# Optimization experiments

Hardware: AMD Instinct MI355X
Metric: run time of the kernel (lower is better)

Reference implementation:

```python
import jax, jax.numpy as jnp
import numpy as np
import math

B, T = 16, 512
P = 256          # num_memory_positions
E = 128          # embedding_dim
NB = 4           # num_beings
K = 4            # attention_radius
TEMP = 8.0       # attention_temperature
PHI = 1.618033988749895


def setup_inputs() -> dict:
    key = jax.random.key(0)
    ks = jax.random.split(key, 8)
    x = jax.random.normal(ks[0], (B, T, 8), jnp.float32)
    W_in = jax.random.normal(ks[1], (8, E), jnp.float32) * 0.1
    b_in = jnp.zeros((E,), jnp.float32)
    W_out = jax.random.normal(ks[2], (E, 8), jnp.float32) * 0.1
    b_out = jnp.zeros((8,), jnp.float32)
    W_p = jax.random.normal(ks[3], (E, E), jnp.float32) * (1.0 / np.sqrt(E))
    b_p = jnp.zeros((E,), jnp.float32)
    ptr_dest = jax.random.uniform(ks[4], (NB, P), jnp.float32) * P
    jump_W = jax.random.normal(ks[5], (NB, E), jnp.float32) * 0.1
    jump_b = jnp.zeros((NB,), jnp.float32)
    ctx_strength = jnp.full((NB,), 0.2, jnp.float32)
    pe = np.zeros((NB, E), np.float32)
    for i in range(NB):
        ph = i * PHI
        v = []
        for h in range(1, 9):
            v += [math.sin(h * ph), math.cos(h * ph)]
        pe[i, :16] = v  # phase_embedding padded with zeros to E (E >= 16)
    phase_bias = jnp.asarray(pe)
    seg = P / NB
    pointer_init = jax.random.uniform(ks[6], (NB, B), jnp.float32) * seg + jnp.arange(NB, dtype=jnp.float32)[:, None] * seg
    return dict(x=x, W_in=W_in, b_in=b_in, W_out=W_out, b_out=b_out,
                W_p=W_p, b_p=b_p, ptr_dest=ptr_dest, jump_W=jump_W,
                jump_b=jump_b, ctx_strength=ctx_strength,
                phase_bias=phase_bias, pointer_init=pointer_init)


def _forward(x, W_in, b_in, W_out, b_out, W_p, b_p, ptr_dest, jump_W,
             jump_b, ctx_strength, phase_bias, pointer_init):
    offsets = jnp.arange(-K, K + 1)          # [W]
    b_ix = jnp.arange(B)                     # [B]
    half = P / 2.0
    ring0 = jnp.zeros((B, P, E), x.dtype)
    hid0 = jnp.zeros((NB, B, E), x.dtype)

    def step(carry, x_t):
        ring, ptrs, hids = carry
        inp = x_t @ W_in + b_in              # [B,E]
        outs, new_ptrs, new_hids = [], [], []
        for i in range(NB):                  # beings sequential (share ring)
            ptr, hid = ptrs[i], hids[i]
            base = jnp.clip(jnp.floor(ptr).astype(jnp.int32), 0, P - 1)
            idx = (base[:, None] + offsets[None, :]) % P            # [B,W]
            delta = jnp.mod(idx.astype(x_t.dtype) - ptr[:, None] + half, P) - half
            w = jax.nn.softmax(-(delta ** 2) / TEMP, axis=1)         # [B,W]
            nbhd = ring[b_ix[:, None], idx]                          # [B,W,E]
            ctx = jnp.sum(w[..., None] * nbhd, axis=1)               # [B,E]
            comb = inp + jax.nn.sigmoid(ctx_strength[i]) * ctx + 0.1 * phase_bias[i]
            s = jnp.tanh(comb + hid)
            s = jnp.tanh(s @ W_p + b_p)      # depth-1 = 1 processing layer
            ring = ring.at[b_ix[:, None], idx].add(w[..., None] * s[:, None, :])
            cur = jnp.clip(ptr.astype(jnp.int32), 0, P - 1)
            jump_target = ptr_dest[i][cur]                           # [B]
            probs = jax.nn.sigmoid(s @ jump_W[i] + jump_b[i])        # [B]
            hard = (probs > 0.5).astype(s.dtype)
            should_jump = hard - jax.lax.stop_gradient(probs) + probs
            walk = (ptr + 1.0) % P
            new_ptrs.append(jnp.where(should_jump > 0.5, jump_target, walk))
            new_hids.append(s)
            outs.append(s @ W_out + b_out)                           # [B,8]
        out_t = jnp.mean(jnp.stack(outs), axis=0)                    # [B,8] (training-mode mean)
        return (ring, jnp.stack(new_ptrs), jnp.stack(new_hids)), out_t

    _, ys = jax.lax.scan(step, (ring0, pointer_init, hid0), jnp.swapaxes(x, 0, 1))
    return jnp.swapaxes(ys, 0, 1)            # [B,T,8]


def reference(x, W_in, b_in, W_out, b_out, W_p, b_p, ptr_dest, jump_W,
              jump_b, ctx_strength, phase_bias, pointer_init):
    return _forward(x, W_in, b_in, W_out, b_out, W_p, b_p, ptr_dest,
                    jump_W, jump_b, ctx_strength, phase_bias, pointer_init)
```

## Files before the change

kernel.cpp:

```cpp
#include <hip/hip_runtime.h>
#include <cmath>

namespace {
constexpr int B_ = 16, T_ = 512, P_ = 256, E_ = 128, NB_ = 4, K_ = 4;

__device__ __forceinline__ float rcpf(float x) { return __builtin_amdgcn_rcpf(x); }
__device__ __forceinline__ float fast_tanh(float x) {
    float a = fabsf(x);
    float t = __expf(-2.0f * a);
    float r = 1.0f - 2.0f * t * rcpf(1.0f + t);
    return copysignf(r, x);
}
__device__ __forceinline__ float redkq(float v) {
    v += __shfl_xor(v, 16);
    v += __shfl_xor(v, 32);
    return v;
}
__device__ __forceinline__ float sel4(int kq, float a, float b, float c, float d) {
    const float t0 = (kq & 1) ? b : a;
    const float t1 = (kq & 1) ? d : c;
    return (kq & 2) ? t1 : t0;
}
}

__global__ __launch_bounds__(256, 1)
void swarm_ring_kernel(const float* __restrict__ x,
                       const float* __restrict__ W_in,
                       const float* __restrict__ b_in,
                       const float* __restrict__ W_out,
                       const float* __restrict__ b_out,
                       const float* __restrict__ W_p,
                       const float* __restrict__ b_p,
                       const float* __restrict__ ptr_dest,
                       const float* __restrict__ jump_W,
                       const float* __restrict__ jump_b,
                       const float* __restrict__ ctx_strength,
                       const float* __restrict__ phase_bias,
                       const float* __restrict__ pointer_init,
                       float* __restrict__ out)
{
    __shared__ alignas(16) float  ring[P_ * E_];
    __shared__ alignas(16) float4 s4[E_];
    __shared__ alignas(16) float  sbuf[2 * E_];
    __shared__ alignas(16) float  red[16];
    __shared__ alignas(16) float  hist[16][132];
    __shared__ alignas(16) float  wout_s[8][132];

    const int tid = threadIdx.x;
    const int b   = blockIdx.x;
    const int w   = tid >> 6;
    const int l   = tid & 63;
    const int sub = l & 15;
    const int kq  = l >> 4;
    const int e0  = ((w << 4) | sub) << 1;

    for (int k4 = tid; k4 < P_ * E_ / 4; k4 += 256)
        ((float4*)ring)[k4] = make_float4(0.f, 0.f, 0.f, 0.f);
    for (int idx = tid; idx < 8 * E_; idx += 256) {
        const int m = idx >> 7, ee = idx & 127;
        wout_s[m][ee] = W_out[ee * 8 + m] * 0.25f;
    }

    float2 wp2[32];
    #pragma unroll
    for (int kk = 0; kk < 32; ++kk)
        wp2[kk] = *(const float2*)(W_p + (kq * 32 + kk) * E_ + e0);

    const float2 bin2 = *(const float2*)(b_in + e0);
    const float2 bp2  = *(const float2*)(b_p + e0);
    const float  bout_m = b_out[tid & 7];

    float2 pb2[NB_], jw2[NB_], hid2[NB_];
    float  sigc[NB_], jb_r[NB_], ptrv[NB_];
    #pragma unroll
    for (int i = 0; i < NB_; ++i) {
        const float2 pb = *(const float2*)(phase_bias + i * E_ + e0);
        pb2[i] = make_float2(0.1f * pb.x, 0.1f * pb.y);
        jw2[i] = *(const float2*)(jump_W + i * E_ + e0);
        sigc[i] = 1.0f / (1.0f + __expf(-ctx_strength[i]));
        jb_r[i] = jump_b[i];
        hid2[i] = make_float2(0.f, 0.f);
        ptrv[i] = pointer_init[i * B_ + b];
    }

    const float* xb = x + (size_t)b * T_ * 8;
    float xt[8];
    {
        float4 a0 = ((const float4*)xb)[0], a1 = ((const float4*)xb)[1];
        xt[0]=a0.x; xt[1]=a0.y; xt[2]=a0.z; xt[3]=a0.w;
        xt[4]=a1.x; xt[5]=a1.y; xt[6]=a1.z; xt[7]=a1.w;
    }

    const float Cw1 = 0.8824969f, Cw2 = 0.60653066f, Cw3 = 0.32465247f, Cw4 = 0.13533528f;
    const float Dw1 = 0.7788008f, Dw2 = 0.36787944f, Dw3 = 0.105399225f, Dw4 = 0.018315639f;

    __syncthreads();

    for (int t = 0; t < T_; ++t) {
        int   baseA[NB_];
        float fA[NB_], psinv[NB_], jt[NB_], wgt[NB_][9];
        #pragma unroll
        for (int i = 0; i < NB_; ++i) {
            const float p = ptrv[i];
            const int base = (int)p;
            baseA[i] = base;
            jt[i] = ptr_dest[i * P_ + base];
            const float f = p - (float)base;
            fA[i] = f;
            const float r  = __expf(0.25f * f);
            const float r2 = r * r, r3 = r2 * r, r4 = r2 * r2;
            const float ri = rcpf(r), ri2 = ri * ri, ri3 = ri2 * ri, ri4 = ri2 * ri2;
            const float p0 = Cw4*ri4, p1 = Cw3*ri3, p2 = Cw2*ri2, p3 = Cw1*ri, p4 = 1.0f,
                        p5 = Cw1*r,  p6 = Cw2*r2,  p7 = Cw3*r3,  p8 = Cw4*r4;
            const float sum = ((p0+p1)+(p2+p3)) + ((p4+p5)+(p6+p7)) + p8;
            const float inv = rcpf(sum);
            psinv[i] = inv;
            wgt[i][0]=p0*inv; wgt[i][1]=p1*inv; wgt[i][2]=p2*inv; wgt[i][3]=p3*inv;
            wgt[i][4]=p4*inv; wgt[i][5]=p5*inv; wgt[i][6]=p6*inv; wgt[i][7]=p7*inv;
            wgt[i][8]=p8*inv;
        }

        int ddm[NB_][NB_];
        bool overlap = false;
        #pragma unroll
        for (int j = 1; j < NB_; ++j)
            #pragma unroll
            for (int i = 0; i < j; ++i) {
                const int dd = ((baseA[j] - baseA[i] + 128) & 255) - 128;
                ddm[j][i] = dd;
                overlap = overlap || (dd >= -8 && dd <= 8);
            }

        float  ws0[NB_], ws1[NB_];
        float2 ctxp2[NB_];
        #pragma unroll
        for (int i = 0; i < NB_; ++i) {
            ws0[i] = sel4(kq, wgt[i][0], wgt[i][1], wgt[i][2], wgt[i][3]);
            ws1[i] = sel4(kq, wgt[i][4], wgt[i][5], wgt[i][6], wgt[i][7]);
            const int r0 = (baseA[i] + kq - K_) & (P_ - 1);
            const int r1 = (baseA[i] + kq + 4 - K_) & (P_ - 1);
            const float2 g0 = *(const float2*)(ring + r0 * E_ + e0);
            const float2 g1 = *(const float2*)(ring + r1 * E_ + e0);
            float cx = fmaf(ws1[i], g1.x, ws0[i] * g0.x);
            float cy = fmaf(ws1[i], g1.y, ws0[i] * g0.y);
            if (kq == 0) {
                const int r2 = (baseA[i] + 8 - K_) & (P_ - 1);
                const float2 g2 = *(const float2*)(ring + r2 * E_ + e0);
                cx = fmaf(wgt[i][8], g2.x, cx);
                cy = fmaf(wgt[i][8], g2.y, cy);
            }
            ctxp2[i] = make_float2(redkq(cx), redkq(cy));
        }

        float2 inp2 = bin2;
        #pragma unroll
        for (int k = 0; k < 8; ++k) {
            const float2 wk = *(const float2*)(W_in + k * E_ + e0);
            inp2.x = fmaf(xt[k], wk.x, inp2.x);
            inp2.y = fmaf(xt[k], wk.y, inp2.y);
        }

        float xtn[8];
        if (t + 1 < T_) {
            float4 a0 = ((const float4*)(xb + (t + 1) * 8))[0];
            float4 a1 = ((const float4*)(xb + (t + 1) * 8))[1];
            xtn[0]=a0.x; xtn[1]=a0.y; xtn[2]=a0.z; xtn[3]=a0.w;
            xtn[4]=a1.x; xtn[5]=a1.y; xtn[6]=a1.z; xtn[7]=a1.w;
        } else {
            #pragma unroll
            for (int k = 0; k < 8; ++k) xtn[k] = 0.f;
        }

        float2 sv2[NB_];

        if (!overlap) {
            float2 s1v[NB_];
            #pragma unroll
            for (int j = 0; j < NB_; ++j) {
                s1v[j].x = fast_tanh(fmaf(sigc[j], ctxp2[j].x, inp2.x + pb2[j].x + hid2[j].x));
                s1v[j].y = fast_tanh(fmaf(sigc[j], ctxp2[j].y, inp2.y + pb2[j].y + hid2[j].y));
            }
            if (kq == 0) {
                s4[e0]     = make_float4(s1v[0].x, s1v[1].x, s1v[2].x, s1v[3].x);
                s4[e0 + 1] = make_float4(s1v[0].y, s1v[1].y, s1v[2].y, s1v[3].y);
            }
            __syncthreads();

            float2 ab0 = make_float2(0.f, 0.f), ab1 = ab0, ab2 = ab0, ab3 = ab0;
            const float4* sp = s4 + kq * 32;
            #pragma unroll
            for (int kk = 0; kk < 32; ++kk) {
                const float4 sq = sp[kk];
                const float2 w2 = wp2[kk];
                ab0.x = fmaf(sq.x, w2.x, ab0.x); ab0.y = fmaf(sq.x, w2.y, ab0.y);
                ab1.x = fmaf(sq.y, w2.x, ab1.x); ab1.y = fmaf(sq.y, w2.y, ab1.y);
                ab2.x = fmaf(sq.z, w2.x, ab2.x); ab2.y = fmaf(sq.z, w2.y, ab2.y);
                ab3.x = fmaf(sq.w, w2.x, ab3.x); ab3.y = fmaf(sq.w, w2.y, ab3.y);
            }
            sv2[0] = make_float2(fast_tanh(redkq(ab0.x) + bp2.x), fast_tanh(redkq(ab0.y) + bp2.y));
            sv2[1] = make_float2(fast_tanh(redkq(ab1.x) + bp2.x), fast_tanh(redkq(ab1.y) + bp2.y));
            sv2[2] = make_float2(fast_tanh(redkq(ab2.x) + bp2.x), fast_tanh(redkq(ab2.y) + bp2.y));
            sv2[3] = make_float2(fast_tanh(redkq(ab3.x) + bp2.x), fast_tanh(redkq(ab3.y) + bp2.y));
            #pragma unroll
            for (int j = 0; j < NB_; ++j) hid2[j] = sv2[j];

            #pragma unroll
            for (int j = 0; j < NB_; ++j) {
                const float2 s = sv2[j];
                const int r0 = (baseA[j] + kq - K_) & (P_ - 1);
                float2* q0 = (float2*)(ring + r0 * E_ + e0);
                float2 v0 = *q0;
                v0.x = fmaf(ws0[j], s.x, v0.x); v0.y = fmaf(ws0[j], s.y, v0.y);
                *q0 = v0;
                const int r1 = (baseA[j] + kq + 4 - K_) & (P_ - 1);
                float2* q1 = (float2*)(ring + r1 * E_ + e0);
                float2 v1 = *q1;
                v1.x = fmaf(ws1[j], s.x, v1.x); v1.y = fmaf(ws1[j], s.y, v1.y);
                *q1 = v1;
                if (kq == 0) {
                    const int r2 = (baseA[j] + 8 - K_) & (P_ - 1);
                    float2* q2 = (float2*)(ring + r2 * E_ + e0);
                    float2 v2 = *q2;
                    v2.x = fmaf(wgt[j][8], s.x, v2.x); v2.y = fmaf(wgt[j][8], s.y, v2.y);
                    *q2 = v2;
                }
            }
        } else {
            float coefm[NB_][NB_];
            #pragma unroll
            for (int j = 1; j < NB_; ++j) {
                #pragma unroll
                for (int i = 0; i < j; ++i) {
                    const int dd = ddm[j][i];
                    float c = 0.f;
                    if (dd >= -8 && dd <= 8) {
                        const float A = (float)dd - fA[i];
                        const float s  = __expf(-0.25f * (A - fA[j]));
                        const float G  = __expf(0.125f * (fA[i] * fA[i] - A * A));
                        const float s2p = s * s, s3p = s2p * s, s4p = s2p * s2p;
                        const float si = rcpf(s), si2 = si * si, si3 = si2 * si, si4 = si2 * si2;
                        float acc = 0.f;
                        acc += (dd >= 0)              ? Dw4 * si4 : 0.f;
                        acc += (dd >= -1 && dd <= 7)  ? Dw3 * si3 : 0.f;
                        acc += (dd >= -2 && dd <= 6)  ? Dw2 * si2 : 0.f;
                        acc += (dd >= -3 && dd <= 5)  ? Dw1 * si  : 0.f;
                        acc += (dd >= -4 && dd <= 4)  ? 1.0f      : 0.f;
                        acc += (dd >= -5 && dd <= 3)  ? Dw1 * s   : 0.f;
                        acc += (dd >= -6 && dd <= 2)  ? Dw2 * s2p : 0.f;
                        acc += (dd >= -7 && dd <= 1)  ? Dw3 * s3p : 0.f;
                        acc += (dd <= 0)              ? Dw4 * s4p : 0.f;
                        c = psinv[i] * psinv[j] * G * acc;
                    }
                    coefm[j][i] = c;
                }
            }

            #pragma unroll
            for (int j = 0; j < NB_; ++j) {
                float2 ctx = ctxp2[j];
                #pragma unroll
                for (int i = 0; i < j; ++i) {
                    ctx.x = fmaf(coefm[j][i], sv2[i].x, ctx.x);
                    ctx.y = fmaf(coefm[j][i], sv2[i].y, ctx.y);
                }
                float2 s1;
                s1.x = fast_tanh(fmaf(sigc[j], ctx.x, inp2.x + pb2[j].x + hid2[j].x));
                s1.y = fast_tanh(fmaf(sigc[j], ctx.y, inp2.y + pb2[j].y + hid2[j].y));
                if (kq == 0) *(float2*)(sbuf + (j & 1) * E_ + e0) = s1;
                __syncthreads();

                const float4* sp = (const float4*)(sbuf + (j & 1) * E_) + kq * 8;
                float ax = 0.f, ay = 0.f;
                #pragma unroll
                for (int kk = 0; kk < 8; ++kk) {
                    const float4 sq = sp[kk];
                    const float2 wa = wp2[4 * kk + 0], wb = wp2[4 * kk + 1];
                    const float2 wc = wp2[4 * kk + 2], wd = wp2[4 * kk + 3];
                    ax = fmaf(sq.x, wa.x, ax); ay = fmaf(sq.x, wa.y, ay);
                    ax = fmaf(sq.y, wb.x, ax); ay = fmaf(sq.y, wb.y, ay);
                    ax = fmaf(sq.z, wc.x, ax); ay = fmaf(sq.z, wc.y, ay);
                    ax = fmaf(sq.w, wd.x, ax); ay = fmaf(sq.w, wd.y, ay);
                }
                float2 s2;
                s2.x = fast_tanh(redkq(ax) + bp2.x);
                s2.y = fast_tanh(redkq(ay) + bp2.y);
                sv2[j] = s2; hid2[j] = s2;

                const int r0 = (baseA[j] + kq - K_) & (P_ - 1);
                float2* q0 = (float2*)(ring + r0 * E_ + e0);
                float2 v0 = *q0;
                v0.x = fmaf(ws0[j], s2.x, v0.x); v0.y = fmaf(ws0[j], s2.y, v0.y);
                *q0 = v0;
                const int r1 = (baseA[j] + kq + 4 - K_) & (P_ - 1);
                float2* q1 = (float2*)(ring + r1 * E_ + e0);
                float2 v1 = *q1;
                v1.x = fmaf(ws1[j], s2.x, v1.x); v1.y = fmaf(ws1[j], s2.y, v1.y);
                *q1 = v1;
                if (kq == 0) {
                    const int r2 = (baseA[j] + 8 - K_) & (P_ - 1);
                    float2* q2 = (float2*)(ring + r2 * E_ + e0);
                    float2 v2 = *q2;
                    v2.x = fmaf(wgt[j][8], s2.x, v2.x); v2.y = fmaf(wgt[j][8], s2.y, v2.y);
                    *q2 = v2;
                }
            }
        }

        {
            float vj0 = fmaf(sv2[0].y, jw2[0].y, sv2[0].x * jw2[0].x);
            float vj1 = fmaf(sv2[1].y, jw2[1].y, sv2[1].x * jw2[1].x);
            float vj2 = fmaf(sv2[2].y, jw2[2].y, sv2[2].x * jw2[2].x);
            float vj3 = fmaf(sv2[3].y, jw2[3].y, sv2[3].x * jw2[3].x);
            #pragma unroll
            for (int off = 1; off < 16; off <<= 1) {
                vj0 += __shfl_xor(vj0, off);
                vj1 += __shfl_xor(vj1, off);
                vj2 += __shfl_xor(vj2, off);
                vj3 += __shfl_xor(vj3, off);
            }
            if (l == 0)
                ((float4*)red)[w] = make_float4(vj0, vj1, vj2, vj3);
        }

        {
            float2 ssum2;
            ssum2.x = (sv2[0].x + sv2[1].x) + (sv2[2].x + sv2[3].x);
            ssum2.y = (sv2[0].y + sv2[1].y) + (sv2[2].y + sv2[3].y);
            if (kq == 0) *(float2*)(&hist[t & 15][e0]) = ssum2;
        }

        __syncthreads();

        {
            const float4 r0 = ((const float4*)red)[0];
            const float4 r1 = ((const float4*)red)[1];
            const float4 r2 = ((const float4*)red)[2];
            const float4 r3 = ((const float4*)red)[3];
            const float zz[4] = {
                ((r0.x + r1.x) + (r2.x + r3.x)) + jb_r[0],
                ((r0.y + r1.y) + (r2.y + r3.y)) + jb_r[1],
                ((r0.z + r1.z) + (r2.z + r3.z)) + jb_r[2],
                ((r0.w + r1.w) + (r2.w + r3.w)) + jb_r[3]};
            #pragma unroll
            for (int i = 0; i < NB_; ++i) {
                float np;
                if (zz[i] > 0.0f) np = jt[i];
                else { np = ptrv[i] + 1.0f; if (np >= 256.0f) np -= 256.0f; }
                ptrv[i] = np;
            }
        }

        if ((t & 7) == 7 && tid < 64) {
            const int tt = tid >> 3;
            const int m  = tid & 7;
            const float* hrow = hist[(t - 7 + tt) & 15];
            const float* wrow = wout_s[m];
            float acc = 0.f;
            #pragma unroll
            for (int q = 0; q < 32; ++q) {
                const float4 h4 = ((const float4*)hrow)[q];
                const float4 w4 = ((const float4*)wrow)[q];
                acc += ((h4.x * w4.x + h4.y * w4.y) + (h4.z * w4.z + h4.w * w4.w));
            }
            out[((size_t)b * T_ + (t - 7 + tt)) * 8 + m] = acc + bout_m;
        }

        #pragma unroll
        for (int k = 0; k < 8; ++k) xt[k] = xtn[k];
    }
}

extern "C" void kernel_launch(void* const* d_in, const int* in_sizes, int n_in,
                              void* d_out, int out_size, void* d_ws, size_t ws_size,
                              hipStream_t stream) {
    (void)in_sizes; (void)n_in; (void)out_size; (void)d_ws; (void)ws_size;
    swarm_ring_kernel<<<dim3(B_), dim3(256), 0, stream>>>(
        (const float*)d_in[0],  (const float*)d_in[1],  (const float*)d_in[2],
        (const float*)d_in[3],  (const float*)d_in[4],  (const float*)d_in[5],
        (const float*)d_in[6],  (const float*)d_in[7],  (const float*)d_in[8],
        (const float*)d_in[9],  (const float*)d_in[10], (const float*)d_in[11],
        (const float*)d_in[12], (float*)d_out);
}
```

Before: 2.058 ms.

## Group beings into dependency levels to batch independent beings per barrier

Replaces the binary overlap/no-overlap split with a dependency-level schedule. Each being gets a level based on which earlier beings' ring windows it overlaps, and all beings in the same level compute their pre-activation and projection together behind one barrier. Partial overlaps no longer force fully sequential processing, which cuts the number of __syncthreads per step. In exchange, the fully independent case loses its specialised four-way batched matvec, adds per-being level branches, and always computes the coupling coefficients.

```diff
diff --git a/kernel.cpp b/kernel.cpp
--- a/kernel.cpp
+++ b/kernel.cpp
@@ -39,12 +39,11 @@
                        const float* __restrict__ pointer_init,
                        float* __restrict__ out)
 {
-    __shared__ alignas(16) float  ring[P_ * E_];
-    __shared__ alignas(16) float4 s4[E_];
-    __shared__ alignas(16) float  sbuf[2 * E_];
-    __shared__ alignas(16) float  red[16];
-    __shared__ alignas(16) float  hist[16][132];
-    __shared__ alignas(16) float  wout_s[8][132];
+    __shared__ alignas(16) float ring[P_ * E_];
+    __shared__ alignas(16) float s1p[NB_ * E_];
+    __shared__ alignas(16) float red[16];
+    __shared__ alignas(16) float hist[16][132];
+    __shared__ alignas(16) float wout_s[8][132];
 
     const int tid = threadIdx.x;
     const int b   = blockIdx.x;
@@ -121,15 +120,22 @@
         }
 
         int ddm[NB_][NB_];
-        bool overlap = false;
-        #pragma unroll
-        for (int j = 1; j < NB_; ++j)
+        int lev[NB_];
+        lev[0] = 0;
+        #pragma unroll
+        for (int j = 1; j < NB_; ++j) {
+            int mx = -1;
             #pragma unroll
             for (int i = 0; i < j; ++i) {
                 const int dd = ((baseA[j] - baseA[i] + 128) & 255) - 128;
                 ddm[j][i] = dd;
-                overlap = overlap || (dd >= -8 && dd <= 8);
-            }
+                if (dd >= -8 && dd <= 8 && lev[i] > mx) mx = lev[i];
+            }
+            lev[j] = mx + 1;
+        }
+        const int nlev = 1 + ((lev[1] > lev[0] ? lev[1] : lev[0]) > (lev[2] > lev[3] ? lev[2] : lev[3])
+                              ? (lev[1] > lev[0] ? lev[1] : lev[0])
+                              : (lev[2] > lev[3] ? lev[2] : lev[3]));
 
         float  ws0[NB_], ws1[NB_];
         float2 ctxp2[NB_];
@@ -152,6 +158,35 @@
             ctxp2[i] = make_float2(redkq(cx), redkq(cy));
         }
 
+        float coefm[NB_][NB_];
+        #pragma unroll
+        for (int j = 1; j < NB_; ++j) {
+            #pragma unroll
+            for (int i = 0; i < j; ++i) {
+                const int dd = ddm[j][i];
+                float c = 0.f;
+                if (dd >= -8 && dd <= 8) {
+                    const float A = (float)dd - fA[i];
+                    const float s  = __expf(-0.25f * (A - fA[j]));
+                    const float G  = __expf(0.125f * (fA[i] * fA[i] - A * A));
+                    const float s2p = s * s, s3p = s2p * s, s4p = s2p * s2p;
+                    const float si = rcpf(s), si2 = si * si, si3 = si2 * si, si4 = si2 * si2;
+                    float acc = 0.f;
+                    acc += (dd >= 0)              ? Dw4 * si4 : 0.f;
+                    acc += (dd >= -1 && dd <= 7)  ? Dw3 * si3 : 0.f;
+                    acc += (dd >= -2 && dd <= 6)  ? Dw2 * si2 : 0.f;
+                    acc += (dd >= -3 && dd <= 5)  ? Dw1 * si  : 0.f;
+                    acc += (dd >= -4 && dd <= 4)  ? 1.0f      : 0.f;
+                    acc += (dd >= -5 && dd <= 3)  ? Dw1 * s   : 0.f;
+                    acc += (dd >= -6 && dd <= 2)  ? Dw2 * s2p : 0.f;
+                    acc += (dd >= -7 && dd <= 1)  ? Dw3 * s3p : 0.f;
+                    acc += (dd <= 0)              ? Dw4 * s4p : 0.f;
+                    c = psinv[i] * psinv[j] * G * acc;
+                }
+                coefm[j][i] = c;
+            }
+        }
+
         float2 inp2 = bin2;
         #pragma unroll
         for (int k = 0; k < 8; ++k) {
@@ -172,91 +207,13 @@
         }
 
         float2 sv2[NB_];
-
-        if (!overlap) {
-            float2 s1v[NB_];
+        #pragma unroll
+        for (int j = 0; j < NB_; ++j) sv2[j] = make_float2(0.f, 0.f);
+
+        for (int L = 0; L < nlev; ++L) {
             #pragma unroll
             for (int j = 0; j < NB_; ++j) {
-                s1v[j].x = fast_tanh(fmaf(sigc[j], ctxp2[j].x, inp2.x + pb2[j].x + hid2[j].x));
-                s1v[j].y = fast_tanh(fmaf(sigc[j], ctxp2[j].y, inp2.y + pb2[j].y + hid2[j].y));
-            }
-            if (kq == 0) {
-                s4[e0]     = make_float4(s1v[0].x, s1v[1].x, s1v[2].x, s1v[3].x);
-                s4[e0 + 1] = make_float4(s1v[0].y, s1v[1].y, s1v[2].y, s1v[3].y);
-            }
-            __syncthreads();
-
-            float2 ab0 = make_float2(0.f, 0.f), ab1 = ab0, ab2 = ab0, ab3 = ab0;
-            const float4* sp = s4 + kq * 32;
-            #pragma unroll
-            for (int kk = 0; kk < 32; ++kk) {
-                const float4 sq = sp[kk];
-                const float2 w2 = wp2[kk];
-                ab0.x = fmaf(sq.x, w2.x, ab0.x); ab0.y = fmaf(sq.x, w2.y, ab0.y);
-                ab1.x = fmaf(sq.y, w2.x, ab1.x); ab1.y = fmaf(sq.y, w2.y, ab1.y);
-                ab2.x = fmaf(sq.z, w2.x, ab2.x); ab2.y = fmaf(sq.z, w2.y, ab2.y);
-                ab3.x = fmaf(sq.w, w2.x, ab3.x); ab3.y = fmaf(sq.w, w2.y, ab3.y);
-            }
-            sv2[0] = make_float2(fast_tanh(redkq(ab0.x) + bp2.x), fast_tanh(redkq(ab0.y) + bp2.y));
-            sv2[1] = make_float2(fast_tanh(redkq(ab1.x) + bp2.x), fast_tanh(redkq(ab1.y) + bp2.y));
-            sv2[2] = make_float2(fast_tanh(redkq(ab2.x) + bp2.x), fast_tanh(redkq(ab2.y) + bp2.y));
-            sv2[3] = make_float2(fast_tanh(redkq(ab3.x) + bp2.x), fast_tanh(redkq(ab3.y) + bp2.y));
-            #pragma unroll
-            for (int j = 0; j < NB_; ++j) hid2[j] = sv2[j];
-
-            #pragma unroll
-            for (int j = 0; j < NB_; ++j) {
-                const float2 s = sv2[j];
-                const int r0 = (baseA[j] + kq - K_) & (P_ - 1);
-                float2* q0 = (float2*)(ring + r0 * E_ + e0);
-                float2 v0 = *q0;
-                v0.x = fmaf(ws0[j], s.x, v0.x); v0.y = fmaf(ws0[j], s.y, v0.y);
-                *q0 = v0;
-                const int r1 = (baseA[j] + kq + 4 - K_) & (P_ - 1);
-                float2* q1 = (float2*)(ring + r1 * E_ + e0);
-                float2 v1 = *q1;
-                v1.x = fmaf(ws1[j], s.x, v1.x); v1.y = fmaf(ws1[j], s.y, v1.y);
-                *q1 = v1;
-                if (kq == 0) {
-                    const int r2 = (baseA[j] + 8 - K_) & (P_ - 1);
-                    float2* q2 = (float2*)(ring + r2 * E_ + e0);
-                    float2 v2 = *q2;
-                    v2.x = fmaf(wgt[j][8], s.x, v2.x); v2.y = fmaf(wgt[j][8], s.y, v2.y);
-                    *q2 = v2;
-                }
-            }
-        } else {
-            float coefm[NB_][NB_];
-            #pragma unroll
-            for (int j = 1; j < NB_; ++j) {
-                #pragma unroll
-                for (int i = 0; i < j; ++i) {
-                    const int dd = ddm[j][i];
-                    float c = 0.f;
-                    if (dd >= -8 && dd <= 8) {
-                        const float A = (float)dd - fA[i];
-                        const float s  = __expf(-0.25f * (A - fA[j]));
-                        const float G  = __expf(0.125f * (fA[i] * fA[i] - A * A));
-                        const float s2p = s * s, s3p = s2p * s, s4p = s2p * s2p;
-                        const float si = rcpf(s), si2 = si * si, si3 = si2 * si, si4 = si2 * si2;
-                        float acc = 0.f;
-                        acc += (dd >= 0)              ? Dw4 * si4 : 0.f;
-                        acc += (dd >= -1 && dd <= 7)  ? Dw3 * si3 : 0.f;
-                        acc += (dd >= -2 && dd <= 6)  ? Dw2 * si2 : 0.f;
-                        acc += (dd >= -3 && dd <= 5)  ? Dw1 * si  : 0.f;
-                        acc += (dd >= -4 && dd <= 4)  ? 1.0f      : 0.f;
-                        acc += (dd >= -5 && dd <= 3)  ? Dw1 * s   : 0.f;
-                        acc += (dd >= -6 && dd <= 2)  ? Dw2 * s2p : 0.f;
-                        acc += (dd >= -7 && dd <= 1)  ? Dw3 * s3p : 0.f;
-                        acc += (dd <= 0)              ? Dw4 * s4p : 0.f;
-                        c = psinv[i] * psinv[j] * G * acc;
-                    }
-                    coefm[j][i] = c;
-                }
-            }
-
-            #pragma unroll
-            for (int j = 0; j < NB_; ++j) {
+                if (lev[j] != L) continue;
                 float2 ctx = ctxp2[j];
                 #pragma unroll
                 for (int i = 0; i < j; ++i) {
@@ -266,10 +223,14 @@
                 float2 s1;
                 s1.x = fast_tanh(fmaf(sigc[j], ctx.x, inp2.x + pb2[j].x + hid2[j].x));
                 s1.y = fast_tanh(fmaf(sigc[j], ctx.y, inp2.y + pb2[j].y + hid2[j].y));
-                if (kq == 0) *(float2*)(sbuf + (j & 1) * E_ + e0) = s1;
-                __syncthreads();
-
-                const float4* sp = (const float4*)(sbuf + (j & 1) * E_) + kq * 8;
+                if (kq == 0) *(float2*)(s1p + j * E_ + e0) = s1;
+            }
+            __syncthreads();
+
+            #pragma unroll
+            for (int j = 0; j < NB_; ++j) {
+                if (lev[j] != L) continue;
+                const float4* sp = (const float4*)(s1p + j * E_) + kq * 8;
                 float ax = 0.f, ay = 0.f;
                 #pragma unroll
                 for (int kk = 0; kk < 8; ++kk) {
```

Measured after the change: 2.060 ms. Within noise of the previous version (+0.1%).
